# Kernel optimization log

Hardware: AMD Instinct MI355X
Metric: run time of the kernel (lower is better)

The kernel has to match this reference:

```python
import jax, jax.numpy as jnp
import numpy as np

B, T, D, H, L, OUT = 16, 48, 256, 8, 3, 6
STYLE, SKILL = 64, 64


def _ln(x, g, b):
    m = jnp.mean(x, -1, keepdims=True)
    v = jnp.mean((x - m) ** 2, -1, keepdims=True)
    return (x - m) * jax.lax.rsqrt(v + 1e-5) * g + b


def _gelu(x):
    return jax.nn.gelu(x, approximate=False)  # torch 'gelu' activation is exact erf form


def _mha(q_in, kv_in, qkv_w, qkv_b, o_w, o_b, mask):
    d = q_in.shape[-1]
    hd = d // H
    wq, wk, wv = jnp.split(qkv_w, 3, 0)
    bq, bk, bv = jnp.split(qkv_b, 3, 0)

    def heads(x, w, b):
        y = x @ w.T + b
        return y.reshape(y.shape[0], y.shape[1], H, hd)

    q, k, v = heads(q_in, wq, bq), heads(kv_in, wk, bk), heads(kv_in, wv, bv)
    s = jnp.einsum('bqhd,bkhd->bhqk', q, k) / np.float32(np.sqrt(hd))
    if mask is not None:
        s = jnp.where(mask, jnp.float32(-1e9), s)
    a = jax.nn.softmax(s, -1)
    o = jnp.einsum('bhqk,bkhd->bqhd', a, v).reshape(q_in.shape[0], q_in.shape[1], d)
    return o @ o_w.T + o_b


def _pos_encoding():
    pos = jnp.arange(T, dtype=jnp.float32)[:, None]
    div = jnp.exp(jnp.arange(0, D, 2, dtype=jnp.float32) * (-np.log(10000.0) / D))
    pe = jnp.zeros((T, D), jnp.float32)
    pe = pe.at[:, 0::2].set(jnp.sin(pos * div))
    pe = pe.at[:, 1::2].set(jnp.cos(pos * div))
    return pe


def setup_inputs() -> dict:
    key = jax.random.key(0)
    ks = iter(jax.random.split(key, 40))

    def rn(shape, s=0.05):
        return jax.random.normal(next(ks), shape, jnp.float32) * s

    return {
        'z_style': jax.random.normal(next(ks), (B, STYLE), jnp.float32),
        'z_skill': jax.random.normal(next(ks), (B, SKILL), jnp.float32),
        'start_token': jnp.zeros((1, 1, OUT), jnp.float32),
        'mem_w1': rn((D, STYLE + SKILL)), 'mem_b1': jnp.zeros((D,), jnp.float32),
        'mem_ln_g': jnp.ones((D,), jnp.float32), 'mem_ln_b': jnp.zeros((D,), jnp.float32),
        'mem_w2': rn((D, D)), 'mem_b2': jnp.zeros((D,), jnp.float32),
        'emb_w': rn((D, OUT)), 'emb_b': jnp.zeros((D,), jnp.float32),
        'sa_qkv_w': rn((L, 3 * D, D)), 'sa_qkv_b': jnp.zeros((L, 3 * D), jnp.float32),
        'sa_o_w': rn((L, D, D)), 'sa_o_b': jnp.zeros((L, D), jnp.float32),
        'ca_qkv_w': rn((L, 3 * D, D)), 'ca_qkv_b': jnp.zeros((L, 3 * D), jnp.float32),
        'ca_o_w': rn((L, D, D)), 'ca_o_b': jnp.zeros((L, D), jnp.float32),
        'ln1_g': jnp.ones((L, D), jnp.float32), 'ln1_b': jnp.zeros((L, D), jnp.float32),
        'ln2_g': jnp.ones((L, D), jnp.float32), 'ln2_b': jnp.zeros((L, D), jnp.float32),
        'ln3_g': jnp.ones((L, D), jnp.float32), 'ln3_b': jnp.zeros((L, D), jnp.float32),
        'ff1_w': rn((L, 4 * D, D)), 'ff1_b': jnp.zeros((L, 4 * D), jnp.float32),
        'ff2_w': rn((L, D, 4 * D)), 'ff2_b': jnp.zeros((L, D), jnp.float32),
        'op_w1': rn((D // 2, D)), 'op_b1': jnp.zeros((D // 2,), jnp.float32),
        'op_w2': rn((OUT, D // 2)), 'op_b2': jnp.zeros((OUT,), jnp.float32),
    }


def reference(z_style, z_skill, start_token, mem_w1, mem_b1, mem_ln_g, mem_ln_b,
              mem_w2, mem_b2, emb_w, emb_b, sa_qkv_w, sa_qkv_b, sa_o_w, sa_o_b,
              ca_qkv_w, ca_qkv_b, ca_o_w, ca_o_b, ln1_g, ln1_b, ln2_g, ln2_b,
              ln3_g, ln3_b, ff1_w, ff1_b, ff2_w, ff2_b, op_w1, op_b1, op_w2, op_b2):
    # memory: [B,1,D] expanded to seq_len (identical rows, as in the torch module)
    cond = jnp.concatenate([z_style, z_skill], -1)
    h = _gelu(_ln(cond @ mem_w1.T + mem_b1, mem_ln_g, mem_ln_b))
    memory = jnp.broadcast_to((h @ mem_w2.T + mem_b2)[:, None, :], (B, T, D))

    pe = _pos_encoding()
    causal = jnp.triu(jnp.ones((T, T), bool), 1)  # True = masked (future)
    layer_ps = (sa_qkv_w, sa_qkv_b, sa_o_w, sa_o_b, ca_qkv_w, ca_qkv_b, ca_o_w,
                ca_o_b, ln1_g, ln1_b, ln2_g, ln2_b, ln3_g, ln3_b,
                ff1_w, ff1_b, ff2_w, ff2_b)

    def layer_step(x, p):
        (sqw, sqb, sow, sob, cqw, cqb, cow, cob, g1, b1, g2, b2, g3, b3,
         f1w, f1b, f2w, f2b) = p
        # post-norm TransformerDecoderLayer (torch default norm_first=False)
        x = _ln(x + _mha(x, x, sqw, sqb, sow, sob, causal), g1, b1)
        x = _ln(x + _mha(x, memory, cqw, cqb, cow, cob, None), g2, b2)
        x = _ln(x + (_gelu(x @ f1w.T + f1b) @ f2w.T + f2b), g3, b3)
        return x, None

    def t_step(inputs, t):
        # Causal mask => decoded[:, t] depends only on inputs[:, :t+1]; running the
        # padded full-length decoder reproduces the torch growing-prefix loop exactly.
        x = inputs @ emb_w.T + emb_b + pe[None]
        dec, _ = jax.lax.scan(layer_step, x, layer_ps)
        d_t = jax.lax.dynamic_slice(dec, (0, t, 0), (B, 1, D))[:, 0]
        out_t = _gelu(d_t @ op_w1.T + op_b1) @ op_w2.T + op_b2
        inputs = jax.lax.dynamic_update_slice(inputs, out_t[:, None, :], (0, t + 1, 0))
        return inputs, out_t

    inputs0 = jnp.zeros((B, T, OUT), jnp.float32).at[:, 0:1, :].set(
        jnp.broadcast_to(start_token, (B, 1, OUT)))
    _, ys = jax.lax.scan(t_step, inputs0, jnp.arange(T))
    return jnp.transpose(ys, (1, 0, 2))  # [B, T, OUT]
```

## Files before the change

### kernel.cpp

```cpp
#include <hip/hip_runtime.h>
#include <hip/hip_bf16.h>
#include <math.h>

#define NGRP 16
#define GWG  8
#define NBLK (NGRP*GWG)
#define NTHR 512
#define TSEQ 48
#define DDIM 256
#define HDIM 32
#define NLAY 3
#define NOUT 6

#define CNT_OFF   0u
#define CNT_BYTES 16384u
#define GRP_OFF   16384u
#define GRP_STRF  5120u
#define PO_F   0
#define PF_F   2048
#define CAL_F  4096
#define WB_OFF 360448u
#define WOFF_QKV 0u
#define WOFF_WO  589824u
#define WOFF_F1  786432u
#define WOFF_F2  1572864u
#define WOFF_OP1 2359296u
#define NCVT     2392064u

typedef __attribute__((address_space(1))) const unsigned int gu32;
typedef __attribute__((address_space(3))) unsigned int lu32;

__device__ __forceinline__ void gl_lds16(const unsigned short* g, unsigned short* l) {
  __builtin_amdgcn_global_load_lds((gu32*)g, (lu32*)l, 16, 0, 0);
}
__device__ __forceinline__ void bfp(unsigned int u, float& lo, float& hi) {
  union { unsigned int i; float f; } a, b;
  a.i = u << 16; b.i = u & 0xffff0000u; lo = a.f; hi = b.f;
}
__device__ __forceinline__ float gelu_exact(float x) {
  return 0.5f * x * (1.0f + erff(x * 0.70710678118654752f));
}
__device__ __forceinline__ float dot8(const uint4& u, const float* x, int k0) {
  float lo, hi, acc = 0.f;
  bfp(u.x, lo, hi); acc += x[k0  ]*lo + x[k0+1]*hi;
  bfp(u.y, lo, hi); acc += x[k0+2]*lo + x[k0+3]*hi;
  bfp(u.z, lo, hi); acc += x[k0+4]*lo + x[k0+5]*hi;
  bfp(u.w, lo, hi); acc += x[k0+6]*lo + x[k0+7]*hi;
  return acc;
}

__global__ void convert_bf16(const float* qkv, const float* ow, const float* f1,
                             const float* f2, const float* w1, unsigned char* ws) {
  __hip_bfloat16* dst = (__hip_bfloat16*)(ws + WB_OFF);
  size_t stride = (size_t)gridDim.x * blockDim.x;
  for (size_t i = (size_t)blockIdx.x * blockDim.x + threadIdx.x; i < NCVT; i += stride) {
    float v;
    if      (i < WOFF_WO)  v = qkv[i];
    else if (i < WOFF_F1)  v = ow[i - WOFF_WO];
    else if (i < WOFF_F2)  v = f1[i - WOFF_F1];
    else if (i < WOFF_OP1) v = f2[i - WOFF_F2];
    else                   v = w1[i - WOFF_OP1];
    dst[i] = __float2bfloat16(v);
  }
}

__global__ void precompute_ca(const float* zs, const float* zk,
                              const float* mw1, const float* mb1,
                              const float* mlg, const float* mlb,
                              const float* mw2, const float* mb2,
                              const float* cqw, const float* cqb,
                              const float* cow, const float* cob,
                              unsigned char* ws) {
  const int g = blockIdx.x & 15, l = blockIdx.x >> 4;
  const int tid = threadIdx.x;
  __shared__ float cond[128], h[256], mvv[256], vv[256], lred[16];

  auto lnstat = [&](float v, float& m, float& rs) {
    float a = v, b = v * v;
    #pragma unroll
    for (int off = 32; off; off >>= 1) { a += __shfl_xor(a, off); b += __shfl_xor(b, off); }
    if ((tid & 63) == 0) { lred[tid >> 6] = a; lred[4 + (tid >> 6)] = b; }
    __syncthreads();
    float sa = lred[0]+lred[1]+lred[2]+lred[3];
    float sb = lred[4]+lred[5]+lred[6]+lred[7];
    m = sa * (1.0f/256.0f);
    rs = rsqrtf(sb * (1.0f/256.0f) - m*m + 1e-5f);
    __syncthreads();
  };

  if (tid < 128) cond[tid] = (tid < 64) ? zs[g*64 + tid] : zk[g*64 + tid - 64];
  __syncthreads();
  float acc = mb1[tid];
  { const float* w = mw1 + (size_t)tid * 128;
    for (int k = 0; k < 128; k += 4) {
      float4 q = *(const float4*)(w + k);
      acc += q.x*cond[k] + q.y*cond[k+1] + q.z*cond[k+2] + q.w*cond[k+3];
    } }
  float m, rs; lnstat(acc, m, rs);
  h[tid] = gelu_exact((acc - m) * rs * mlg[tid] + mlb[tid]);
  __syncthreads();
  float a2 = mb2[tid];
  { const float* w = mw2 + (size_t)tid * 256;
    for (int k = 0; k < 256; k += 4) {
      float4 q = *(const float4*)(w + k);
      a2 += q.x*h[k] + q.y*h[k+1] + q.z*h[k+2] + q.w*h[k+3];
    } }
  mvv[tid] = a2;
  __syncthreads();
  float a3 = cqb[l*768 + 512 + tid];
  { const float* w = cqw + ((size_t)l*768 + 512 + tid) * 256;
    for (int k = 0; k < 256; k += 4) {
      float4 q = *(const float4*)(w + k);
      a3 += q.x*mvv[k] + q.y*mvv[k+1] + q.z*mvv[k+2] + q.w*mvv[k+3];
    } }
  vv[tid] = a3;
  __syncthreads();
  float a4 = cob[l*256 + tid];
  { const float* w = cow + ((size_t)l*256 + tid) * 256;
    for (int k = 0; k < 256; k += 4) {
      float4 q = *(const float4*)(w + k);
      a4 += q.x*vv[k] + q.y*vv[k+1] + q.z*vv[k+2] + q.w*vv[k+3];
    } }
  ((float*)(ws + GRP_OFF))[(size_t)g * GRP_STRF + CAL_F + l*256 + tid] = a4;
}

struct DecP {
  const float *start_token, *emb_w, *emb_b;
  const float *sa_qkv_b, *sa_o_b;
  const float *ln1_g, *ln1_b, *ln2_g, *ln2_b, *ln3_g, *ln3_b;
  const float *ff1_b, *ff2_b;
  const float *op_b1, *op_w2, *op_b2;
  float* out;
  unsigned char* ws;
};

__global__ __launch_bounds__(NTHR, 1) void decoder_persistent(DecP p) {
  const int g = blockIdx.x >> 3;
  const int s = blockIdx.x & 7;
  const int tid = threadIdx.x;

  unsigned int* flg = (unsigned int*)(p.ws + CNT_OFF) + (size_t)g * 256;
  float* grp = (float*)(p.ws + GRP_OFF) + (size_t)g * GRP_STRF;
  float* Po = grp + PO_F;
  float* Pf = grp + PF_F;
  const float* CALW = grp + CAL_F;
  const unsigned short* WB = (const unsigned short*)(p.ws + WB_OFF);

  __shared__ __align__(16) unsigned short Rws[32768];
  __shared__ float xls[DDIM], x2ls[DDIM], red[NTHR], lred[32], fxl[128];
  __shared__ float qb[HDIM], ah[HDIM], sc[64];
  __shared__ float kc[NLAY*TSEQ*33], vc[NLAY*TSEQ*33];
  __shared__ float cals[768], obias[768], ff2b[768];
  __shared__ float ln1g[768], ln1b[768], ln2g[768], ln2b[768], ln3g[768], ln3b[768];
  __shared__ float qkvb[288], ff1b[384];
  __shared__ float embw[DDIM*NOUT], embb[DDIM];
  __shared__ float opb1[128], opw2[NOUT*128], opb2[8], OUTV[8];

  const int row = tid >> 2, kk = tid & 3;
  const int wv = tid >> 6, ln = tid & 63;

  auto stage_qkv = [&](int l) {
    #pragma unroll
    for (int r = 0; r < 6; ++r) {
      int c = (r*8 + wv)*64 + ln;
      int rw = c >> 5, wc = (c & 31) ^ (rw & 7);
      const unsigned short* gp = WB + WOFF_QKV
        + ((size_t)(l*768 + (rw>>5)*256 + s*32 + (rw&31)))*256 + wc*8;
      gl_lds16(gp, Rws + (size_t)(r*8 + wv)*512);
    }
  };
  auto stage_ff1 = [&](int l) {
    #pragma unroll
    for (int r = 0; r < 8; ++r) {
      int c = (r*8 + wv)*64 + ln;
      int rw = c >> 5, wc = (c & 31) ^ (rw & 7);
      const unsigned short* gp = WB + WOFF_F1
        + ((size_t)(l*1024 + s*128 + rw))*256 + wc*8;
      gl_lds16(gp, Rws + (size_t)(r*8 + wv)*512);
    }
  };
  auto stage_ff2 = [&](int l) {
    #pragma unroll
    for (int r = 0; r < 8; ++r) {
      int c = (r*8 + wv)*64 + ln;
      int rw = c >> 4, wc = (c & 15) ^ (rw & 15);
      const unsigned short* gp = WB + WOFF_F2
        + ((size_t)(l*256 + rw))*1024 + s*128 + wc*8;
      gl_lds16(gp, Rws + (size_t)(r*8 + wv)*512);
    }
  };

  uint4 pWO[4], pO1[8];
  auto ldWO = [&](int l) {
    if (tid < 256) {
      const unsigned short* w = WB + WOFF_WO + ((size_t)(l*256 + tid))*256 + s*32;
      #pragma unroll
      for (int c = 0; c < 4; ++c) pWO[c] = *(const uint4*)(w + c*8);
    }
  };
  auto ldO1 = [&]() {
    const unsigned short* w = WB + WOFF_OP1 + (size_t)row*256 + kk*64;
    #pragma unroll
    for (int i = 0; i < 8; ++i) pO1[i] = *(const uint4*)(w + i*8);
  };

  unsigned int barcount = 0;
  auto gbar = [&]() {
    __syncthreads();
    ++barcount;
    if (tid == 0)
      __hip_atomic_store(flg + s*32, barcount, __ATOMIC_RELEASE, __HIP_MEMORY_SCOPE_AGENT);
    if (tid < GWG) {
      while (__hip_atomic_load(flg + tid*32, __ATOMIC_RELAXED, __HIP_MEMORY_SCOPE_AGENT) < barcount) {}
    }
    if (tid == 0)
      (void)__hip_atomic_load(flg + s*32, __ATOMIC_ACQUIRE, __HIP_MEMORY_SCOPE_AGENT);
    __syncthreads();
  };

  auto lnstats = [&](float v, float* slot, float& m, float& rs) {
    float a = v, b = v * v;
    #pragma unroll
    for (int off = 32; off; off >>= 1) { a += __shfl_xor(a, off); b += __shfl_xor(b, off); }
    if ((tid & 63) == 0 && tid < 256) { slot[tid >> 6] = a; slot[4 + (tid >> 6)] = b; }
    __syncthreads();
    float sa = slot[0]+slot[1]+slot[2]+slot[3];
    float sb = slot[4]+slot[5]+slot[6]+slot[7];
    m = sa * (1.0f/256.0f);
    rs = rsqrtf(sb * (1.0f/256.0f) - m*m + 1e-5f);
  };

  for (int i = tid; i < 768; i += NTHR) {
    cals[i]  = CALW[i];
    obias[i] = p.sa_o_b[i];
    ff2b[i]  = p.ff2_b[i];
    ln1g[i] = p.ln1_g[i]; ln1b[i] = p.ln1_b[i];
    ln2g[i] = p.ln2_g[i]; ln2b[i] = p.ln2_b[i];
    ln3g[i] = p.ln3_g[i]; ln3b[i] = p.ln3_b[i];
  }
  for (int i = tid; i < 288; i += NTHR) {
    int l = i / 96, r = i % 96, sect = (r >> 5), o = r & 31;
    qkvb[i] = p.sa_qkv_b[l*768 + sect*256 + s*32 + o];
  }
  for (int i = tid; i < 384; i += NTHR) {
    int l = i >> 7, o = i & 127;
    ff1b[i] = p.ff1_b[l*1024 + s*128 + o];
  }
  for (int i = tid; i < DDIM*NOUT; i += NTHR) embw[i] = p.emb_w[i];
  for (int i = tid; i < DDIM; i += NTHR) embb[i] = p.emb_b[i];
  for (int i = tid; i < 128; i += NTHR) opb1[i] = p.op_b1[i];
  for (int i = tid; i < NOUT*128; i += NTHR) opw2[i] = p.op_w2[i];
  if (tid < NOUT) OUTV[tid] = p.start_token[tid];
  if (tid < 8) opb2[tid] = (tid < NOUT) ? p.op_b2[tid] : 0.f;

  const float divv = (tid < 256) ? expf(-0.035977892078031968f * (float)(2*(tid>>1))) : 0.f;
  __syncthreads();

  if (tid < 256) {
    float acc = embb[tid] + ((tid & 1) ? 1.0f : 0.0f);
    #pragma unroll
    for (int j = 0; j < NOUT; ++j) acc += OUTV[j] * embw[tid*NOUT + j];
    xls[tid] = acc;
  }
  stage_qkv(0);
  ldWO(0);
  __syncthreads();

  for (int t = 0; t < TSEQ; ++t) {
    for (int l = 0; l < NLAY; ++l) {
      if (l > 0) {
        float r2 = 0.f;
        if (tid < 256) {
          r2 = x2ls[tid] + ff2b[(l-1)*256 + tid];
          #pragma unroll
          for (int ss = 0; ss < GWG; ++ss) r2 += Pf[ss*256 + tid];
        }
        float m, rs; lnstats(r2, lred + 0, m, rs);
        if (tid < 256)
          xls[tid] = (r2 - m) * rs * ln3g[(l-1)*256 + tid] + ln3b[(l-1)*256 + tid];
        __syncthreads();
      }
      if (row < 96) {
        float acc = 0.f;
        #pragma unroll
        for (int i = 0; i < 8; ++i) {
          int ii = (i + kk) & 7;
          int k0 = kk*64 + ii*8;
          const uint4 w = *(const uint4*)(Rws + row*256 + (k0 ^ ((row&7)<<3)));
          acc += dot8(w, xls, k0);
        }
        acc += __shfl_xor(acc, 1);
        acc += __shfl_xor(acc, 2);
        if (kk == 0) {
          float v = acc + qkvb[l*96 + row];
          int sect = row >> 5, o = row & 31;
          if (sect == 0) qb[o] = v;
          else if (sect == 1) kc[(l*TSEQ + t)*33 + o] = v;
          else vc[(l*TSEQ + t)*33 + o] = v;
        }
      }
      __syncthreads();
      stage_ff1(l);
      if (tid < 64) {
        float scj = -1e30f;
        if (tid <= t) {
          const float* kr = &kc[(l*TSEQ + tid)*33];
          float a = 0.f;
          #pragma unroll
          for (int d = 0; d < HDIM; ++d) a += qb[d] * kr[d];
          scj = a * 0.17677669529663687f;
        }
        float mx = scj;
        #pragma unroll
        for (int off = 32; off; off >>= 1) mx = fmaxf(mx, __shfl_xor(mx, off));
        float e = (tid <= t) ? expf(scj - mx) : 0.f;
        float su = e;
        #pragma unroll
        for (int off = 32; off; off >>= 1) su += __shfl_xor(su, off);
        sc[tid] = e / su;
      }
      __syncthreads();
      if (tid < 256) {
        int d = tid >> 3, jg = tid & 7;
        float acc = 0.f;
        for (int j = jg; j <= t; j += 8) acc += sc[j] * vc[(l*TSEQ + j)*33 + d];
        acc += __shfl_xor(acc, 1);
        acc += __shfl_xor(acc, 2);
        acc += __shfl_xor(acc, 4);
        if (jg == 0) ah[d] = acc;
      }
      __syncthreads();
      if (tid < 256) {
        float acc = 0.f;
        #pragma unroll
        for (int c = 0; c < 4; ++c) acc += dot8(pWO[c], ah, c*8);
        Po[s*256 + tid] = acc;
      }
      gbar();

      float r = 0.f;
      if (tid < 256) {
        r = xls[tid] + obias[l*256 + tid];
        #pragma unroll
        for (int ss = 0; ss < GWG; ++ss) r += Po[ss*256 + tid];
      }
      float m1, rs1; lnstats(r, lred + 8, m1, rs1);
      float z = 0.f;
      if (tid < 256)
        z = (r - m1)*rs1*ln1g[l*256 + tid] + ln1b[l*256 + tid] + cals[l*256 + tid];
      float m2, rs2; lnstats(z, lred + 16, m2, rs2);
      if (tid < 256) x2ls[tid] = (z - m2)*rs2*ln2g[l*256 + tid] + ln2b[l*256 + tid];
      __syncthreads();
      float facc = 0.f;
      {
        #pragma unroll
        for (int i = 0; i < 8; ++i) {
          int ii = (i + kk) & 7;
          int k0 = kk*64 + ii*8;
          const uint4 w = *(const uint4*)(Rws + row*256 + (k0 ^ ((row&7)<<3)));
          facc += dot8(w, x2ls, k0);
        }
        facc += __shfl_xor(facc, 1);
        facc += __shfl_xor(facc, 2);
      }
      __syncthreads();
      stage_ff2(l);
      if (kk == 0) fxl[row] = gelu_exact(facc + ff1b[l*128 + row]);
      __syncthreads();
      if (tid < 256) {
        float acc2 = 0.f;
        #pragma unroll
        for (int j2 = 0; j2 < 16; ++j2) {
          int k0 = j2*8;
          const uint4 w = *(const uint4*)(Rws + tid*128 + (k0 ^ ((tid&15)<<3)));
          acc2 += dot8(w, fxl, k0);
        }
        Pf[s*256 + tid] = acc2;
      }
      __syncthreads();
      {
        int lnx = (l == 2) ? 0 : l + 1;
        stage_qkv(lnx);
        ldWO(lnx);
        if (l == 2) ldO1();
      }
      gbar();
    }

    {
      float r2 = 0.f;
      if (tid < 256) {
        r2 = x2ls[tid] + ff2b[2*256 + tid];
        #pragma unroll
        for (int ss = 0; ss < GWG; ++ss) r2 += Pf[ss*256 + tid];
      }
      float m, rs; lnstats(r2, lred + 24, m, rs);
      if (tid < 256) xls[tid] = (r2 - m)*rs*ln3g[2*256 + tid] + ln3b[2*256 + tid];
      __syncthreads();
      float oacc = 0.f;
      #pragma unroll
      for (int i = 0; i < 8; ++i) oacc += dot8(pO1[i], xls, kk*64 + i*8);
      oacc += __shfl_xor(oacc, 1);
      oacc += __shfl_xor(oacc, 2);
      if (kk == 0) fxl[row] = gelu_exact(oacc + opb1[row]);
      __syncthreads();
      if (tid < 192) {
        int oo = tid >> 5, kl = tid & 31;
        float acc = fxl[kl]*opw2[oo*128 + kl] + fxl[kl+32]*opw2[oo*128 + kl+32]
                  + fxl[kl+64]*opw2[oo*128 + kl+64] + fxl[kl+96]*opw2[oo*128 + kl+96];
        #pragma unroll
        for (int off = 16; off; off >>= 1) acc += __shfl_xor(acc, off);
        if (kl == 0) {
          float v = acc + opb2[oo];
          OUTV[oo] = v;
          if (s == 0) p.out[((size_t)g*TSEQ + t)*NOUT + oo] = v;
        }
      }
      __syncthreads();
      if (tid < 256) {
        float ang = (float)(t + 1) * divv;
        float pe = (tid & 1) ? cosf(ang) : sinf(ang);
        float acc = embb[tid] + pe;
        #pragma unroll
        for (int j = 0; j < NOUT; ++j) acc += OUTV[j] * embw[tid*NOUT + j];
        xls[tid] = acc;
      }
      __syncthreads();
    }
  }
}

extern "C" void kernel_launch(void* const* d_in, const int* in_sizes, int n_in,
                              void* d_out, int out_size, void* d_ws, size_t ws_size,
                              hipStream_t stream) {
  const float* const* F = (const float* const*)d_in;
  const float* z_style = F[0]; const float* z_skill = F[1];
  DecP p;
  p.start_token = F[2];
  const float* mem_w1 = F[3]; const float* mem_b1 = F[4];
  const float* mem_ln_g = F[5]; const float* mem_ln_b = F[6];
  const float* mem_w2 = F[7]; const float* mem_b2 = F[8];
  p.emb_w = F[9]; p.emb_b = F[10];
  const float* sa_qkv_w = F[11]; p.sa_qkv_b = F[12];
  const float* sa_o_w  = F[13]; p.sa_o_b = F[14];
  const float* ca_qkv_w = F[15]; const float* ca_qkv_b = F[16];
  const float* ca_o_w = F[17]; const float* ca_o_b = F[18];
  p.ln1_g = F[19]; p.ln1_b = F[20]; p.ln2_g = F[21]; p.ln2_b = F[22];
  p.ln3_g = F[23]; p.ln3_b = F[24];
  const float* ff1_w = F[25]; p.ff1_b = F[26];
  const float* ff2_w = F[27]; p.ff2_b = F[28];
  const float* op_w1 = F[29]; p.op_b1 = F[30]; p.op_w2 = F[31]; p.op_b2 = F[32];
  p.out = (float*)d_out;
  p.ws  = (unsigned char*)d_ws;

  hipMemsetAsync((char*)d_ws + CNT_OFF, 0, CNT_BYTES, stream);
  convert_bf16<<<dim3(512), dim3(256), 0, stream>>>(sa_qkv_w, sa_o_w, ff1_w, ff2_w, op_w1,
                                                    (unsigned char*)d_ws);
  precompute_ca<<<dim3(48), dim3(256), 0, stream>>>(z_style, z_skill, mem_w1, mem_b1,
                                                    mem_ln_g, mem_ln_b, mem_w2, mem_b2,
                                                    ca_qkv_w, ca_qkv_b, ca_o_w, ca_o_b,
                                                    (unsigned char*)d_ws);
  decoder_persistent<<<dim3(NBLK), dim3(NTHR), 0, stream>>>(p);
}
```

Measured before the change: 2.334 ms.

## Process two batch elements per workgroup group to reuse staged weights

Halves the grid from 16 groups to 8, so each 8-block group now decodes two batch elements at once. Each staged weight row in LDS or registers is applied to both elements' activations, which halves total weight traffic and the number of blocks spinning on global barriers. The KV cache is stored as bf16 in LDS so both elements fit. Partial sums move to a new exchange region. This adds per-block work, lowers parallelism across CUs, and the bf16 K/V storage adds rounding error.

```diff
diff --git a/kernel.cpp b/kernel.cpp
--- a/kernel.cpp
+++ b/kernel.cpp
@@ -2,9 +2,9 @@
 #include <hip/hip_bf16.h>
 #include <math.h>
 
-#define NGRP 16
+#define NGRP2 8
 #define GWG  8
-#define NBLK (NGRP*GWG)
+#define NBLK (NGRP2*GWG)
 #define NTHR 512
 #define TSEQ 48
 #define DDIM 256
@@ -13,11 +13,9 @@
 #define NOUT 6
 
 #define CNT_OFF   0u
-#define CNT_BYTES 16384u
+#define CNT_BYTES 8192u
 #define GRP_OFF   16384u
 #define GRP_STRF  5120u
-#define PO_F   0
-#define PF_F   2048
 #define CAL_F  4096
 #define WB_OFF 360448u
 #define WOFF_QKV 0u
@@ -26,6 +24,7 @@
 #define WOFF_F2  1572864u
 #define WOFF_OP1 2359296u
 #define NCVT     2392064u
+#define EXCH_OFF 5505024u
 
 typedef __attribute__((address_space(1))) const unsigned int gu32;
 typedef __attribute__((address_space(3))) unsigned int lu32;
@@ -36,6 +35,13 @@
 __device__ __forceinline__ void bfp(unsigned int u, float& lo, float& hi) {
   union { unsigned int i; float f; } a, b;
   a.i = u << 16; b.i = u & 0xffff0000u; lo = a.f; hi = b.f;
+}
+__device__ __forceinline__ float bf2f(unsigned short u) {
+  union { unsigned int i; float f; } c; c.i = ((unsigned int)u) << 16; return c.f;
+}
+__device__ __forceinline__ unsigned short f2bf(float f) {
+  __hip_bfloat16 h = __float2bfloat16(f);
+  union { __hip_bfloat16 h; unsigned short u; } c; c.h = h; return c.u;
 }
 __device__ __forceinline__ float gelu_exact(float x) {
   return 0.5f * x * (1.0f + erff(x * 0.70710678118654752f));
@@ -135,28 +141,30 @@
 };
 
 __global__ __launch_bounds__(NTHR, 1) void decoder_persistent(DecP p) {
-  const int g = blockIdx.x >> 3;
-  const int s = blockIdx.x & 7;
+  const int gg = blockIdx.x & 7;
+  const int s = blockIdx.x >> 3;
   const int tid = threadIdx.x;
 
-  unsigned int* flg = (unsigned int*)(p.ws + CNT_OFF) + (size_t)g * 256;
-  float* grp = (float*)(p.ws + GRP_OFF) + (size_t)g * GRP_STRF;
-  float* Po = grp + PO_F;
-  float* Pf = grp + PF_F;
-  const float* CALW = grp + CAL_F;
+  unsigned int* flg = (unsigned int*)(p.ws + CNT_OFF) + (size_t)gg * 256;
+  float* EX = (float*)(p.ws + EXCH_OFF) + (size_t)gg * 8192;
+  float* PoG = EX;
+  float* PfG = EX + 4096;
+  const float* GRPW = (const float*)(p.ws + GRP_OFF);
   const unsigned short* WB = (const unsigned short*)(p.ws + WB_OFF);
 
   __shared__ __align__(16) unsigned short Rws[32768];
-  __shared__ float xls[DDIM], x2ls[DDIM], red[NTHR], lred[32], fxl[128];
-  __shared__ float qb[HDIM], ah[HDIM], sc[64];
-  __shared__ float kc[NLAY*TSEQ*33], vc[NLAY*TSEQ*33];
-  __shared__ float cals[768], obias[768], ff2b[768];
+  __shared__ __align__(16) unsigned short kcb[2][NLAY*TSEQ*34];
+  __shared__ __align__(16) unsigned short vcb[2][NLAY*TSEQ*34];
+  __shared__ float xls[2][DDIM], x2ls[2][DDIM], lred[64], fxl[2][128];
+  __shared__ float qb[2][HDIM], ah[2][HDIM], sc[2][64];
+  __shared__ float cals[2*768], obias[768], ff2b[768];
   __shared__ float ln1g[768], ln1b[768], ln2g[768], ln2b[768], ln3g[768], ln3b[768];
   __shared__ float qkvb[288], ff1b[384];
   __shared__ float embw[DDIM*NOUT], embb[DDIM];
-  __shared__ float opb1[128], opw2[NOUT*128], opb2[8], OUTV[8];
+  __shared__ float opb1[128], opw2[NOUT*128], opb2[8], OUTV[2][8];
 
   const int row = tid >> 2, kk = tid & 3;
+  const int el = tid >> 8, tl = tid & 255;
   const int wv = tid >> 6, ln = tid & 63;
 
   auto stage_qkv = [&](int l) {
@@ -192,11 +200,9 @@
 
   uint4 pWO[4], pO1[8];
   auto ldWO = [&](int l) {
-    if (tid < 256) {
-      const unsigned short* w = WB + WOFF_WO + ((size_t)(l*256 + tid))*256 + s*32;
-      #pragma unroll
-      for (int c = 0; c < 4; ++c) pWO[c] = *(const uint4*)(w + c*8);
-    }
+    const unsigned short* w = WB + WOFF_WO + ((size_t)(l*256 + tl))*256 + s*32;
+    #pragma unroll
+    for (int c = 0; c < 4; ++c) pWO[c] = *(const uint4*)(w + c*8);
   };
   auto ldO1 = [&]() {
     const unsigned short* w = WB + WOFF_OP1 + (size_t)row*256 + kk*64;
@@ -222,22 +228,26 @@
     float a = v, b = v * v;
     #pragma unroll
     for (int off = 32; off; off >>= 1) { a += __shfl_xor(a, off); b += __shfl_xor(b, off); }
-    if ((tid & 63) == 0 && tid < 256) { slot[tid >> 6] = a; slot[4 + (tid >> 6)] = b; }
+    if (ln == 0) { slot[wv] = a; slot[8 + wv] = b; }
     __syncthreads();
-    float sa = slot[0]+slot[1]+slot[2]+slot[3];
-    float sb = slot[4]+slot[5]+slot[6]+slot[7];
+    int b0 = el*4;
+    float sa = slot[b0]+slot[b0+1]+slot[b0+2]+slot[b0+3];
+    float sb = slot[8+b0]+slot[9+b0]+slot[10+b0]+slot[11+b0];
     m = sa * (1.0f/256.0f);
     rs = rsqrtf(sb * (1.0f/256.0f) - m*m + 1e-5f);
   };
 
   for (int i = tid; i < 768; i += NTHR) {
-    cals[i]  = CALW[i];
     obias[i] = p.sa_o_b[i];
     ff2b[i]  = p.ff2_b[i];
     ln1g[i] = p.ln1_g[i]; ln1b[i] = p.ln1_b[i];
     ln2g[i] = p.ln2_g[i]; ln2b[i] = p.ln2_b[i];
     ln3g[i] = p.ln3_g[i]; ln3b[i] = p.ln3_b[i];
   }
+  for (int i = tid; i < 2*768; i += NTHR) {
+    int eh = i / 768;
+    cals[i] = GRPW[(size_t)(gg*2 + eh) * GRP_STRF + CAL_F + (i % 768)];
+  }
   for (int i = tid; i < 288; i += NTHR) {
     int l = i / 96, r = i % 96, sect = (r >> 5), o = r & 31;
     qkvb[i] = p.sa_qkv_b[l*768 + sect*256 + s*32 + o];
@@ -250,17 +260,17 @@
   for (int i = tid; i < DDIM; i += NTHR) embb[i] = p.emb_b[i];
   for (int i = tid; i < 128; i += NTHR) opb1[i] = p.op_b1[i];
   for (int i = tid; i < NOUT*128; i += NTHR) opw2[i] = p.op_w2[i];
-  if (tid < NOUT) OUTV[tid] = p.start_token[tid];
+  if (tl < NOUT) OUTV[el][tl] = p.start_token[tl];
   if (tid < 8) opb2[tid] = (tid < NOUT) ? p.op_b2[tid] : 0.f;
 
-  const float divv = (tid < 256) ? expf(-0.035977892078031968f * (float)(2*(tid>>1))) : 0.f;
-  __syncthreads();
-
-  if (tid < 256) {
-    float acc = embb[tid] + ((tid & 1) ? 1.0f : 0.0f);
-    #pragma unroll
-    for (int j = 0; j < NOUT; ++j) acc += OUTV[j] * embw[tid*NOUT + j];
-    xls[tid] = acc;
+  const float divv = expf(-0.035977892078031968f * (float)(2*(tl>>1)));
+  __syncthreads();
+
+  {
+    float acc = embb[tl] + ((tl & 1) ? 1.0f : 0.0f);
+    #pragma unroll
+    for (int j = 0; j < NOUT; ++j) acc += OUTV[el][j] * embw[tl*NOUT + j];
+    xls[el][tl] = acc;
   }
   stage_qkv(0);
   ldWO(0);
@@ -269,113 +279,122 @@
   for (int t = 0; t < TSEQ; ++t) {
     for (int l = 0; l < NLAY; ++l) {
       if (l > 0) {
-        float r2 = 0.f;
-        if (tid < 256) {
-          r2 = x2ls[tid] + ff2b[(l-1)*256 + tid];
-          #pragma unroll
-          for (int ss = 0; ss < GWG; ++ss) r2 += Pf[ss*256 + tid];
-        }
+        float r2 = x2ls[el][tl] + ff2b[(l-1)*256 + tl];
+        #pragma unroll
+        for (int ss = 0; ss < GWG; ++ss) r2 += PfG[el*2048 + ss*256 + tl];
         float m, rs; lnstats(r2, lred + 0, m, rs);
-        if (tid < 256)
-          xls[tid] = (r2 - m) * rs * ln3g[(l-1)*256 + tid] + ln3b[(l-1)*256 + tid];
+        xls[el][tl] = (r2 - m) * rs * ln3g[(l-1)*256 + tl] + ln3b[(l-1)*256 + tl];
         __syncthreads();
       }
       if (row < 96) {
-        float acc = 0.f;
+        float aA = 0.f, aB = 0.f;
         #pragma unroll
         for (int i = 0; i < 8; ++i) {
           int ii = (i + kk) & 7;
           int k0 = kk*64 + ii*8;
           const uint4 w = *(const uint4*)(Rws + row*256 + (k0 ^ ((row&7)<<3)));
-          acc += dot8(w, xls, k0);
-        }
-        acc += __shfl_xor(acc, 1);
-        acc += __shfl_xor(acc, 2);
+          aA += dot8(w, xls[0], k0);
+          aB += dot8(w, xls[1], k0);
+        }
+        aA += __shfl_xor(aA, 1); aA += __shfl_xor(aA, 2);
+        aB += __shfl_xor(aB, 1); aB += __shfl_xor(aB, 2);
         if (kk == 0) {
-          float v = acc + qkvb[l*96 + row];
+          float bq = qkvb[l*96 + row];
+          float vA = aA + bq, vB = aB + bq;
           int sect = row >> 5, o = row & 31;
-          if (sect == 0) qb[o] = v;
-          else if (sect == 1) kc[(l*TSEQ + t)*33 + o] = v;
-          else vc[(l*TSEQ + t)*33 + o] = v;
+          if (sect == 0) { qb[0][o] = vA; qb[1][o] = vB; }
+          else if (sect == 1) {
+            kcb[0][(l*TSEQ + t)*34 + o] = f2bf(vA);
+            kcb[1][(l*TSEQ + t)*34 + o] = f2bf(vB);
+          } else {
+            vcb[0][(l*TSEQ + t)*34 + o] = f2bf(vA);
+            vcb[1][(l*TSEQ + t)*34 + o] = f2bf(vB);
+          }
         }
       }
       __syncthreads();
       stage_ff1(l);
-      if (tid < 64) {
+      if (wv < 2) {
+        int ee = wv, j = ln;
         float scj = -1e30f;
-        if (tid <= t) {
-          const float* kr = &kc[(l*TSEQ + tid)*33];
+        if (j <= t) {
+          const unsigned short* kr = &kcb[ee][(l*TSEQ + j)*34];
           float a = 0.f;
           #pragma unroll
-          for (int d = 0; d < HDIM; ++d) a += qb[d] * kr[d];
+          for (int c = 0; c < 16; ++c) {
+            unsigned int u = *(const unsigned int*)(kr + c*2);
+            float lo, hi; bfp(u, lo, hi);
+            a += lo*qb[ee][2*c] + hi*qb[ee][2*c + 1];
+          }
           scj = a * 0.17677669529663687f;
         }
         float mx = scj;
         #pragma unroll
         for (int off = 32; off; off >>= 1) mx = fmaxf(mx, __shfl_xor(mx, off));
-        float e = (tid <= t) ? expf(scj - mx) : 0.f;
+        float e = (j <= t) ? expf(scj - mx) : 0.f;
         float su = e;
         #pragma unroll
         for (int off = 32; off; off >>= 1) su += __shfl_xor(su, off);
-        sc[tid] = e / su;
-      }
-      __syncthreads();
-      if (tid < 256) {
-        int d = tid >> 3, jg = tid & 7;
+        sc[ee][j] = e / su;
+      }
+      __syncthreads();
+      {
+        int d = tl >> 3, jg = tl & 7;
         float acc = 0.f;
-        for (int j = jg; j <= t; j += 8) acc += sc[j] * vc[(l*TSEQ + j)*33 + d];
+        for (int j = jg; j <= t; j += 8)
+          acc += sc[el][j] * bf2f(vcb[el][(l*TSEQ + j)*34 + d]);
         acc += __shfl_xor(acc, 1);
         acc += __shfl_xor(acc, 2);
         acc += __shfl_xor(acc, 4);
-        if (jg == 0) ah[d] = acc;
-      }
-      __syncthreads();
-      if (tid < 256) {
+        if (jg == 0) ah[el][d] = acc;
+      }
+      __syncthreads();
+      {
         float acc = 0.f;
         #pragma unroll
-        for (int c = 0; c < 4; ++c) acc += dot8(pWO[c], ah, c*8);
-        Po[s*256 + tid] = acc;
+        for (int c = 0; c < 4; ++c) acc += dot8(pWO[c], ah[el], c*8);
+        PoG[el*2048 + s*256 + tl] = acc;
       }
       gbar();
 
-      float r = 0.f;
-      if (tid < 256) {
-        r = xls[tid] + obias[l*256 + tid];
-        #pragma unroll
-        for (int ss = 0; ss < GWG; ++ss) r += Po[ss*256 + tid];
-      }
-      float m1, rs1; lnstats(r, lred + 8, m1, rs1);
-      float z = 0.f;
-      if (tid < 256)
-        z = (r - m1)*rs1*ln1g[l*256 + tid] + ln1b[l*256 + tid] + cals[l*256 + tid];
-      float m2, rs2; lnstats(z, lred + 16, m2, rs2);
-      if (tid < 256) x2ls[tid] = (z - m2)*rs2*ln2g[l*256 + tid] + ln2b[l*256 + tid];
-      __syncthreads();
-      float facc = 0.f;
-      {
+      float r = xls[el][tl] + obias[l*256 + tl];
+      #pragma unroll
+      for (int ss = 0; ss < GWG; ++ss) r += PoG[el*2048 + ss*256 + tl];
+      float m1, rs1; lnstats(r, lred + 16, m1, rs1);
+      float z = (r - m1)*rs1*ln1g[l*256 + tl] + ln1b[l*256 + tl] + cals[el*768 + l*256 + tl];
+      float m2, rs2; lnstats(z, lred + 32, m2, rs2);
+      x2ls[el][tl] = (z - m2)*rs2*ln2g[l*256 + tl] + ln2b[l*256 + tl];
+      __syncthreads();
+      {
+        float aA = 0.f, aB = 0.f;
         #pragma unroll
         for (int i = 0; i < 8; ++i) {
           int ii = (i + kk) & 7;
           int k0 = kk*64 + ii*8;
           const uint4 w = *(const uint4*)(Rws + row*256 + (k0 ^ ((row&7)<<3)));
-          facc += dot8(w, x2ls, k0);
-        }
-        facc += __shfl_xor(facc, 1);
-        facc += __shfl_xor(facc, 2);
-      }
-      __syncthreads();
-      stage_ff2(l);
-      if (kk == 0) fxl[row] = gelu_exact(facc + ff1b[l*128 + row]);
-      __syncthreads();
-      if (tid < 256) {
+          aA += dot8(w, x2ls[0], k0);
+          aB += dot8(w, x2ls[1], k0);
+        }
+        aA += __shfl_xor(aA, 1); aA += __shfl_xor(aA, 2);
+        aB += __shfl_xor(aB, 1); aB += __shfl_xor(aB, 2);
+        __syncthreads();
+        stage_ff2(l);
+        if (kk == 0) {
+          float bf = ff1b[l*128 + row];
+          fxl[0][row] = gelu_exact(aA + bf);
+          fxl[1][row] = gelu_exact(aB + bf);
+        }
+      }
+      __syncthreads();
+      {
         float acc2 = 0.f;
         #pragma unroll
         for (int j2 = 0; j2 < 16; ++j2) {
           int k0 = j2*8;
-          const uint4 w = *(const uint4*)(Rws + tid*128 + (k0 ^ ((tid&15)<<3)));
-          acc2 += dot8(w, fxl, k0);
-        }
-        Pf[s*256 + tid] = acc2;
+          const uint4 w = *(const uint4*)(Rws + tl*128 + (k0 ^ ((tl&15)<<3)));
+          acc2 += dot8(w, fxl[el], k0);
+        }
+        PfG[el*2048 + s*256 + tl] = acc2;
       }
       __syncthreads();
       {
@@ -388,42 +407,48 @@
     }
 
     {
-      float r2 = 0.f;
-      if (tid < 256) {
-        r2 = x2ls[tid] + ff2b[2*256 + tid];
-        #pragma unroll
-        for (int ss = 0; ss < GWG; ++ss) r2 += Pf[ss*256 + tid];
-      }
-      float m, rs; lnstats(r2, lred + 24, m, rs);
-      if (tid < 256) xls[tid] = (r2 - m)*rs*ln3g[2*256 + tid] + ln3b[2*256 + tid];
-      __syncthreads();
-      float oacc = 0.f;
+      float r2 = x2ls[el][tl] + ff2b[2*256 + tl];
       #pragma unroll
-      for (int i = 0; i < 8; ++i) oacc += dot8(pO1[i], xls, kk*64 + i*8);
-      oacc += __shfl_xor(oacc, 1);
-      oacc += __shfl_xor(oacc, 2);
-      if (kk == 0) fxl[row] = gelu_exact(oacc + opb1[row]);
-      __syncthreads();
-      if (tid < 192) {
-        int oo = tid >> 5, kl = tid & 31;
-        float acc = fxl[kl]*opw2[oo*128 + kl] + fxl[kl+32]*opw2[oo*128 + kl+32]
-                  + fxl[kl+64]*opw2[oo*128 + kl+64] + fxl[kl+96]*opw2[oo*128 + kl+96];
+      for (int ss = 0; ss < GWG; ++ss) r2 += PfG[el*2048 + ss*256 + tl];
+      float m, rs; lnstats(r2, lred + 48, m, rs);
+      xls[el][tl] = (r2 - m)*rs*ln3g[2*256 + tl] + ln3b[2*256 + tl];
+      __syncthreads();
+      {
+        float aA = 0.f, aB = 0.f;
+        #pragma unroll
+        for (int i = 0; i < 8; ++i) {
+          aA += dot8(pO1[i], xls[0], kk*64 + i*8);
+          aB += dot8(pO1[i], xls[1], kk*64 + i*8);
+        }
+        aA += __shfl_xor(aA, 1); aA += __shfl_xor(aA, 2);
+        aB += __shfl_xor(aB, 1); aB += __shfl_xor(aB, 2);
+        if (kk == 0) {
+          float bo = opb1[row];
+          fxl[0][row] = gelu_exact(aA + bo);
+          fxl[1][row] = gelu_exact(aB + bo);
+        }
+      }
+      __syncthreads();
+      if (tl < 192) {
+        int oo = tl >> 5, kl = tl & 31;
+        float acc = fxl[el][kl]*opw2[oo*128 + kl] + fxl[el][kl+32]*opw2[oo*128 + kl+32]
+                  + fxl[el][kl+64]*opw2[oo*128 + kl+64] + fxl[el][kl+96]*opw2[oo*128 + kl+96];
         #pragma unroll
         for (int off = 16; off; off >>= 1) acc += __shfl_xor(acc, off);
         if (kl == 0) {
           float v = acc + opb2[oo];
-          OUTV[oo] = v;
-          if (s == 0) p.out[((size_t)g*TSEQ + t)*NOUT + oo] = v;
-        }
-      }
-      __syncthreads();
-      if (tid < 256) {
+          OUTV[el][oo] = v;
+          if (s == 0) p.out[((size_t)(gg*2 + el)*TSEQ + t)*NOUT + oo] = v;
+        }
+      }
+      __syncthreads();
+      {
         float ang = (float)(t + 1) * divv;
-        float pe = (tid & 1) ? cosf(ang) : sinf(ang);
-        float acc = embb[tid] + pe;
-        #pragma unroll
-        for (int j = 0; j < NOUT; ++j) acc += OUTV[j] * embw[tid*NOUT + j];
-        xls[tid] = acc;
+        float pe = (tl & 1) ? cosf(ang) : sinf(ang);
+        float acc = embb[tl] + pe;
+        #pragma unroll
+        for (int j = 0; j < NOUT; ++j) acc += OUTV[el][j] * embw[tl*NOUT + j];
+        xls[el][tl] = acc;
       }
       __syncthreads();
     }
```

Result: slower. 2.709 ms, median of 2 (+16.0%).
